# Kernel tuning notes

Measured on AMD Instinct MI355X. Metric: run time of the kernel, lower is better.

## Reference

```python
import jax, jax.numpy as jnp
import numpy as np

VOCAB = 100000
DIM = 512
N_POS = 4096
N_NEG = 4096
N_NEU = 2048
CONSISTENCY_WEIGHT = 0.5
SPARSITY_WEIGHT = 0.1


def setup_inputs() -> dict:
    key = jax.random.key(0)
    ks = jax.random.split(key, 7)
    embeddings = jax.random.normal(ks[0], (VOCAB, DIM), dtype=jnp.float32)
    pos_ids = jax.random.randint(ks[1], (N_POS,), 0, VOCAB, dtype=jnp.int64 if jax.config.jax_enable_x64 else jnp.int32)
    pos_dims = jax.random.randint(ks[2], (N_POS,), 0, DIM, dtype=pos_ids.dtype)
    neg_ids = jax.random.randint(ks[3], (N_NEG,), 0, VOCAB, dtype=pos_ids.dtype)
    neg_dims = jax.random.randint(ks[4], (N_NEG,), 0, DIM, dtype=pos_ids.dtype)
    neu_ids = jax.random.randint(ks[5], (N_NEU,), 0, VOCAB, dtype=pos_ids.dtype)
    neu_dims = jax.random.randint(ks[6], (N_NEU,), 0, DIM, dtype=pos_ids.dtype)
    return {"embeddings": embeddings, "pos_ids": pos_ids, "pos_dims": pos_dims,
            "neg_ids": neg_ids, "neg_dims": neg_dims, "neu_ids": neu_ids, "neu_dims": neu_dims}


def _signed_class_loss(embeddings, word_ids, dim_ids, positive: bool):
    # Gather the full embedding rows once; each constraint reads one row.  [N, D]
    vecs = embeddings[word_ids]
    t = jnp.take_along_axis(vecs, dim_ids[:, None], axis=1)[:, 0]  # target-dim values [N]
    abs_t = jnp.abs(t)
    if positive:
        # wrong sign (t<=0): |t|+0.1 penalty; right sign: small reward -0.1*t
        sign_loss = jnp.where(t <= 0, abs_t + 0.1, -t * 0.1)
    else:
        # wrong sign (t>=0): |t|+0.1 penalty; right sign: -0.1*|t| reward
        sign_loss = jnp.where(t >= 0, abs_t + 0.1, -abs_t * 0.1)
    # mean(|vec[other_dims]|) == (sum|vec| - |t|) / (D-1)
    D = embeddings.shape[1]
    sparsity = SPARSITY_WEIGHT * (jnp.sum(jnp.abs(vecs), axis=1) - abs_t) / (D - 1)
    return jnp.sum(sign_loss + sparsity)


def reference(embeddings, pos_ids, pos_dims, neg_ids, neg_dims, neu_ids, neu_dims):
    pos_loss = _signed_class_loss(embeddings, pos_ids, pos_dims, positive=True)
    neg_loss = _signed_class_loss(embeddings, neg_ids, neg_dims, positive=False)
    # neutral: 2*|v[word, dim]|; only the target entry is read
    neu_vals = embeddings[neu_ids, neu_dims]
    neu_loss = jnp.sum(2.0 * jnp.abs(neu_vals))
    num_constraints = pos_ids.shape[0] + neg_ids.shape[0] + neu_ids.shape[0]
    total = pos_loss + neg_loss + neu_loss
    return CONSISTENCY_WEIGHT * (total / num_constraints)
```

## Files before the change

kernel.cpp:

```cpp
#include <hip/hip_runtime.h>


#define DCL_DIM   512
#define DCL_NPOS  4096
#define DCL_NNEG  4096
#define DCL_NNEU  2048
#define DCL_NSIGNED (DCL_NPOS + DCL_NNEG)
#define DCL_NCON  (DCL_NPOS + DCL_NNEG + DCL_NNEU)
#define DCL_SIGNED_BLOCKS (DCL_NSIGNED / 4)
#define DCL_NEU_BLOCKS    (DCL_NNEU / 256)
#define DCL_GRID  (DCL_SIGNED_BLOCKS + DCL_NEU_BLOCKS)

__global__ __launch_bounds__(256) void dcl_main(
    const float* __restrict__ emb,
    const int*   __restrict__ pos_ids, const int* __restrict__ pos_dims,
    const int*   __restrict__ neg_ids, const int* __restrict__ neg_dims,
    const int*   __restrict__ neu_ids, const int* __restrict__ neu_dims,
    float* __restrict__ acc)
{
    const int lane = threadIdx.x & 63;
    const int wv   = threadIdx.x >> 6;

    float contrib = 0.0f;

    if (blockIdx.x < DCL_SIGNED_BLOCKS) {
        const int c = blockIdx.x * 4 + wv;
        const bool is_pos = (c < DCL_NPOS);
        int id, dim;
        if (is_pos) { id = pos_ids[c];            dim = pos_dims[c]; }
        else        { id = neg_ids[c - DCL_NPOS]; dim = neg_dims[c - DCL_NPOS]; }

        const float*  row = emb + (size_t)id * DCL_DIM;
        const float4* r4  = (const float4*)row;

        const float4 a = r4[lane];
        const float4 b = r4[lane + 64];

        float s = fabsf(a.x) + fabsf(a.y) + fabsf(a.z) + fabsf(a.w)
                + fabsf(b.x) + fabsf(b.y) + fabsf(b.z) + fabsf(b.w);

        #pragma unroll
        for (int o = 32; o >= 1; o >>= 1)
            s += __shfl_down(s, o, 64);

        if (lane == 0) {
            const float t  = row[dim];
            const float at = fabsf(t);
            float sign_loss;
            if (is_pos) sign_loss = (t <= 0.0f) ? (at + 0.1f) : (-0.1f * t);
            else        sign_loss = (t >= 0.0f) ? (at + 0.1f) : (-0.1f * at);
            const float sparsity = 0.1f * (s - at) * (1.0f / 511.0f);
            contrib = sign_loss + sparsity;
        }
    } else {
        const int idx = (blockIdx.x - DCL_SIGNED_BLOCKS) * 256 + threadIdx.x;
        const int id  = neu_ids[idx];
        const int dim = neu_dims[idx];
        const float v = emb[(size_t)id * DCL_DIM + dim];
        contrib = 2.0f * fabsf(v);
    }

    #pragma unroll
    for (int o = 32; o >= 1; o >>= 1)
        contrib += __shfl_down(contrib, o, 64);

    __shared__ float sm[4];
    if (lane == 0) sm[wv] = contrib;
    __syncthreads();
    if (threadIdx.x == 0)
        atomicAdd(acc, sm[0] + sm[1] + sm[2] + sm[3]);
}

__global__ void dcl_final(const float* __restrict__ acc, float* __restrict__ out)
{
    if (threadIdx.x == 0)
        out[0] = 0.5f * acc[0] * (1.0f / (float)DCL_NCON);
}

extern "C" void kernel_launch(void* const* d_in, const int* in_sizes, int n_in,
                              void* d_out, int out_size, void* d_ws, size_t ws_size,
                              hipStream_t stream)
{
    const float* emb      = (const float*)d_in[0];
    const int*   pos_ids  = (const int*)d_in[1];
    const int*   pos_dims = (const int*)d_in[2];
    const int*   neg_ids  = (const int*)d_in[3];
    const int*   neg_dims = (const int*)d_in[4];
    const int*   neu_ids  = (const int*)d_in[5];
    const int*   neu_dims = (const int*)d_in[6];

    float* acc = (float*)d_ws;
    hipMemsetAsync(acc, 0, sizeof(float), stream);

    dcl_main<<<DCL_GRID, 256, 0, stream>>>(emb, pos_ids, pos_dims,
                                           neg_ids, neg_dims,
                                           neu_ids, neu_dims, acc);
    dcl_final<<<1, 64, 0, stream>>>(acc, (float*)d_out);
}
```

Baseline: 272.4 us.

## Replace atomic accumulation with per-wave partials and a single reduce kernel

Each wave now writes its own partial sum to workspace, and a single-block kernel reduces them and applies the final scaling. This removes the memset, the per-block atomicAdd and the block-level shared-memory sync in the main kernel. The target element is now pulled from the row already loaded in registers via a lane shuffle, which avoids a dependent scalar global load. The cost is an extra pass over roughly 10k partials in one block.

Measured after the change: 251.9 us (median of 2 runs). -7.5%, faster.

```diff
diff --git a/kernel.cpp b/kernel.cpp
--- a/kernel.cpp
+++ b/kernel.cpp
@@ -5,23 +5,23 @@
 #define DCL_NPOS  4096
 #define DCL_NNEG  4096
 #define DCL_NNEU  2048
-#define DCL_NSIGNED (DCL_NPOS + DCL_NNEG)
 #define DCL_NCON  (DCL_NPOS + DCL_NNEG + DCL_NNEU)
-#define DCL_SIGNED_BLOCKS (DCL_NSIGNED / 4)
+#define DCL_SIGNED_BLOCKS ((DCL_NPOS + DCL_NNEG) / 4)
 #define DCL_NEU_BLOCKS    (DCL_NNEU / 256)
 #define DCL_GRID  (DCL_SIGNED_BLOCKS + DCL_NEU_BLOCKS)
+#define DCL_NPART (DCL_GRID * 4)
 
 __global__ __launch_bounds__(256) void dcl_main(
     const float* __restrict__ emb,
     const int*   __restrict__ pos_ids, const int* __restrict__ pos_dims,
     const int*   __restrict__ neg_ids, const int* __restrict__ neg_dims,
     const int*   __restrict__ neu_ids, const int* __restrict__ neu_dims,
-    float* __restrict__ acc)
+    float* __restrict__ partials)
 {
     const int lane = threadIdx.x & 63;
     const int wv   = threadIdx.x >> 6;
 
-    float contrib = 0.0f;
+    float contrib;
 
     if (blockIdx.x < DCL_SIGNED_BLOCKS) {
         const int c = blockIdx.x * 4 + wv;
@@ -30,51 +30,60 @@
         if (is_pos) { id = pos_ids[c];            dim = pos_dims[c]; }
         else        { id = neg_ids[c - DCL_NPOS]; dim = neg_dims[c - DCL_NPOS]; }
 
-        const float*  row = emb + (size_t)id * DCL_DIM;
-        const float4* r4  = (const float4*)row;
+        const float4* r4 = (const float4*)(emb + (size_t)id * DCL_DIM);
 
         const float4 a = r4[lane];
         const float4 b = r4[lane + 64];
 
+        const int comp = dim & 3;
+        const float ca = (comp == 0) ? a.x : (comp == 1) ? a.y : (comp == 2) ? a.z : a.w;
+        const float cb = (comp == 0) ? b.x : (comp == 1) ? b.y : (comp == 2) ? b.z : b.w;
+        const float cand = (dim < 256) ? ca : cb;
+        const float t = __shfl(cand, (dim >> 2) & 63, 64);
+
         float s = fabsf(a.x) + fabsf(a.y) + fabsf(a.z) + fabsf(a.w)
                 + fabsf(b.x) + fabsf(b.y) + fabsf(b.z) + fabsf(b.w);
-
         #pragma unroll
         for (int o = 32; o >= 1; o >>= 1)
             s += __shfl_down(s, o, 64);
 
-        if (lane == 0) {
-            const float t  = row[dim];
-            const float at = fabsf(t);
-            float sign_loss;
-            if (is_pos) sign_loss = (t <= 0.0f) ? (at + 0.1f) : (-0.1f * t);
-            else        sign_loss = (t >= 0.0f) ? (at + 0.1f) : (-0.1f * at);
-            const float sparsity = 0.1f * (s - at) * (1.0f / 511.0f);
-            contrib = sign_loss + sparsity;
-        }
+        const float at = fabsf(t);
+        float sign_loss;
+        if (is_pos) sign_loss = (t <= 0.0f) ? (at + 0.1f) : (-0.1f * t);
+        else        sign_loss = (t >= 0.0f) ? (at + 0.1f) : (-0.1f * at);
+        contrib = sign_loss + 0.1f * (s - at) * (1.0f / 511.0f);
     } else {
         const int idx = (blockIdx.x - DCL_SIGNED_BLOCKS) * 256 + threadIdx.x;
-        const int id  = neu_ids[idx];
-        const int dim = neu_dims[idx];
-        const float v = emb[(size_t)id * DCL_DIM + dim];
-        contrib = 2.0f * fabsf(v);
+        const float v = emb[(size_t)neu_ids[idx] * DCL_DIM + neu_dims[idx]];
+        float c2 = 2.0f * fabsf(v);
+        #pragma unroll
+        for (int o = 32; o >= 1; o >>= 1)
+            c2 += __shfl_down(c2, o, 64);
+        contrib = c2;
     }
+
+    if (lane == 0)
+        partials[blockIdx.x * 4 + wv] = contrib;
+}
+
+__global__ __launch_bounds__(256) void dcl_reduce(
+    const float* __restrict__ partials, float* __restrict__ out)
+{
+    float s = 0.0f;
+    for (int i = threadIdx.x; i < DCL_NPART; i += 256)
+        s += partials[i];
 
     #pragma unroll
     for (int o = 32; o >= 1; o >>= 1)
-        contrib += __shfl_down(contrib, o, 64);
+        s += __shfl_down(s, o, 64);
 
     __shared__ float sm[4];
-    if (lane == 0) sm[wv] = contrib;
+    const int lane = threadIdx.x & 63;
+    const int wv   = threadIdx.x >> 6;
+    if (lane == 0) sm[wv] = s;
     __syncthreads();
     if (threadIdx.x == 0)
-        atomicAdd(acc, sm[0] + sm[1] + sm[2] + sm[3]);
-}
-
-__global__ void dcl_final(const float* __restrict__ acc, float* __restrict__ out)
-{
-    if (threadIdx.x == 0)
-        out[0] = 0.5f * acc[0] * (1.0f / (float)DCL_NCON);
+        out[0] = (sm[0] + sm[1] + sm[2] + sm[3]) * (0.5f / (float)DCL_NCON);
 }
 
 extern "C" void kernel_launch(void* const* d_in, const int* in_sizes, int n_in,
@@ -89,11 +98,10 @@
     const int*   neu_ids  = (const int*)d_in[5];
     const int*   neu_dims = (const int*)d_in[6];
 
-    float* acc = (float*)d_ws;
-    hipMemsetAsync(acc, 0, sizeof(float), stream);
+    float* partials = (float*)d_ws;
 
     dcl_main<<<DCL_GRID, 256, 0, stream>>>(emb, pos_ids, pos_dims,
                                            neg_ids, neg_dims,
-                                           neu_ids, neu_dims, acc);
-    dcl_final<<<1, 64, 0, stream>>>(acc, (float*)d_out);
+                                           neu_ids, neu_dims, partials);
+    dcl_reduce<<<1, 256, 0, stream>>>(partials, (float*)d_out);
 }
```
